# Kernel optimization log

Hardware: AMD Instinct MI355X
Metric: run time of the kernel (lower is better)

Reference implementation:

```python
import jax, jax.numpy as jnp
import numpy as np

DIM = 512
HEADS = 16
DHEAD = DIM // HEADS
SQRT_DIM = float(np.sqrt(DIM))


def sinusoidal_pe(length, dim):
    # Transformer-XL style sinusoidal positional embedding, shape (length, dim)
    pos = jnp.arange(length, dtype=jnp.float32)[:, None]
    i = jnp.arange(0, dim, 2, dtype=jnp.float32)
    div = jnp.exp(-(jnp.log(jnp.float32(10000.0)) * i / dim))[None, :]
    ang = pos * div
    pe = jnp.zeros((length, dim), dtype=jnp.float32)
    pe = pe.at[:, 0::2].set(jnp.sin(ang)).at[:, 1::2].set(jnp.cos(ang))
    return pe


def rel_shift(x):
    # x: (B, H, L, M) -> Transformer-XL relative shift
    B, H, L, M = x.shape
    x = jnp.concatenate([jnp.zeros((B, H, L, 1), x.dtype), x], axis=-1)  # (B,H,L,M+1)
    x = x.reshape(B, H, M + 1, L)[:, :, 1:, :].reshape(B, H, L, M)
    return x


def setup_inputs() -> dict:
    key = jax.random.key(0)
    ks = jax.random.split(key, 16)
    B, L = 8, 1024
    s = 0.02
    return {
        "query": jax.random.normal(ks[0], (B, L, DIM), jnp.float32),
        "key_in": jax.random.normal(ks[1], (B, L, DIM), jnp.float32),
        "value": jax.random.normal(ks[2], (B, L, DIM), jnp.float32),
        "Wq": jax.random.normal(ks[3], (DIM, DIM), jnp.float32) * s,
        "bq": jnp.zeros((DIM,), jnp.float32),
        "Wk": jax.random.normal(ks[4], (DIM, DIM), jnp.float32) * s,
        "bk": jnp.zeros((DIM,), jnp.float32),
        "Wv": jax.random.normal(ks[5], (DIM, DIM), jnp.float32) * s,
        "bv": jnp.zeros((DIM,), jnp.float32),
        "Wpos": jax.random.normal(ks[6], (DIM, DIM), jnp.float32) * s,
        "u_bias": jax.random.normal(ks[7], (HEADS, DHEAD), jnp.float32) * s,
        "v_bias": jax.random.normal(ks[8], (HEADS, DHEAD), jnp.float32) * s,
        "Wo": jax.random.normal(ks[9], (DIM, DIM), jnp.float32) * s,
        "bo": jnp.zeros((DIM,), jnp.float32),
    }


def reference(query, key_in, value, Wq, bq, Wk, bk, Wv, bv, Wpos, u_bias, v_bias, Wo, bo):
    B, L, _ = value.shape
    pe = sinusoidal_pe(L, DIM)                                   # (L, dim)
    q = (query @ Wq.T + bq).reshape(B, L, HEADS, DHEAD)          # (B,L,H,d)
    k = (key_in @ Wk.T + bk).reshape(B, L, HEADS, DHEAD)         # (B,L,H,d)
    v = (value @ Wv.T + bv).reshape(B, L, HEADS, DHEAD)          # (B,L,H,d)
    pos = (pe @ Wpos.T).reshape(L, HEADS, DHEAD)                 # (L,H,d)

    content_score = jnp.einsum("blhd,bmhd->bhlm", q + u_bias, k)
    pos_score = jnp.einsum("blhd,mhd->bhlm", q + v_bias, pos)
    pos_score = rel_shift(pos_score)
    score = (content_score + pos_score) / SQRT_DIM               # (B,H,L,L)
    attn = jax.nn.softmax(score, axis=-1)
    context = jnp.einsum("bhlm,bmhd->blhd", attn, v).reshape(B, L, DIM)
    return context @ Wo.T + bo
```

## Files before the change

kernel.cpp:

```cpp
#include <hip/hip_runtime.h>
#include <hip/hip_bf16.h>
#include <cstddef>

typedef _Float16 f16;
typedef _Float16 f16x8 __attribute__((ext_vector_type(8)));
typedef _Float16 f16x4 __attribute__((ext_vector_type(4)));
typedef _Float16 f16x2 __attribute__((ext_vector_type(2)));
typedef float    f32x4 __attribute__((ext_vector_type(4)));

#define MFMA16(a,b,c) __builtin_amdgcn_mfma_f32_16x16x32_f16((a),(b),(c),0,0,0)

__device__ __forceinline__ void gload16(const void* g, void* lds) {
  __builtin_amdgcn_global_load_lds((const __attribute__((address_space(1))) void*)g,
                                   (__attribute__((address_space(3))) void*)lds, 16, 0, 0);
}

__global__ __launch_bounds__(256) void conv_w(
    const float* __restrict__ w0, const float* __restrict__ w1,
    const float* __restrict__ w2, const float* __restrict__ w3,
    const float* __restrict__ w4, f16* __restrict__ dst)
{
  const int idx = blockIdx.x * 256 + threadIdx.x;
  const int seg = idx >> 16;
  const int r   = idx & 65535;
  const float* s = seg == 0 ? w0 : seg == 1 ? w1 : seg == 2 ? w2 : seg == 3 ? w3 : w4;
  float4 v = ((const float4*)s)[r];
  f16x4 h = { (f16)v.x, (f16)v.y, (f16)v.z, (f16)v.w };
  ((f16x4*)(dst + ((size_t)seg << 18)))[r] = h;
}

__global__ __launch_bounds__(256) void pe16_kernel(f16* __restrict__ pe) {
  const int l = blockIdx.x;
  const int p = threadIdx.x;
  const float divv = expf(-(logf(10000.0f) * (2.0f * (float)p)) / 512.0f);
  const float ang  = (float)l * divv;
  f16x2 o = { (f16)sinf(ang), (f16)cosf(ang) };
  *(f16x2*)(pe + (size_t)l * 512 + 2 * p) = o;
}

__global__ __launch_bounds__(256) void gemm128_qkv(
    const float* __restrict__ q_in, const float* __restrict__ k_in,
    const float* __restrict__ v_in, const f16* __restrict__ W16,
    const float* __restrict__ bq, const float* __restrict__ bk,
    const float* __restrict__ bv,
    f16* __restrict__ Qf, f16* __restrict__ Kf, f16* __restrict__ Vtf)
{
  __shared__ __align__(16) char Asm[16384];
  __shared__ __align__(16) char Bsm[16384];

  const int z = blockIdx.z;
  const float* Ap   = z == 0 ? q_in : z == 1 ? k_in : v_in;
  const f16*   Wf   = W16 + (size_t)z * 262144;
  const float* bias = z == 0 ? bq : z == 1 ? bk : bv;
  f16*         Cp   = z == 0 ? Qf : z == 1 ? Kf : Vtf;

  const int tid   = threadIdx.x;
  const int gm0   = blockIdx.x * 128;
  const int gn0   = blockIdx.y * 128;
  const int lane  = tid & 63, w = tid >> 6;
  const int row16 = lane & 15, grp = lane >> 4;
  const int wm = w & 1, wn = w >> 1;
  const int lr8  = lane >> 3;
  const int swcb = ((lane & 7) ^ lr8) * 16;

  f32x4 acc[4][4];
#pragma unroll
  for (int i = 0; i < 4; ++i)
#pragma unroll
    for (int j = 0; j < 4; ++j)
#pragma unroll
      for (int r = 0; r < 4; ++r) acc[i][j][r] = 0.f;

  for (int k0 = 0; k0 < 512; k0 += 64) {
    __syncthreads();
    float4 areg[8];
#pragma unroll
    for (int i = 0; i < 8; ++i) {
      const int u = tid + i * 256;
      const int row = u >> 4, cf = (u & 15) * 4;
      areg[i] = *(const float4*)(Ap + (size_t)(gm0 + row) * 512 + k0 + cf);
    }
#pragma unroll
    for (int i = 0; i < 4; ++i) {
      const int rB = w * 32 + i * 8;
      gload16((const char*)Wf + ((size_t)(gn0 + rB + lr8)) * 1024 + (size_t)k0 * 2 + swcb,
              Bsm + rB * 128);
    }
#pragma unroll
    for (int i = 0; i < 8; ++i) {
      const int u = tid + i * 256;
      const int row = u >> 4, cf = (u & 15) * 4;
      f16x4 hv = { (f16)areg[i].x, (f16)areg[i].y, (f16)areg[i].z, (f16)areg[i].w };
      *(f16x4*)(Asm + row * 128 + ((cf * 2) ^ ((row & 7) * 16))) = hv;
    }
    asm volatile("s_waitcnt vmcnt(0)" ::: "memory");
    __syncthreads();
#pragma unroll
    for (int kk = 0; kk < 64; kk += 32) {
      const int cb = (kk + 8 * grp) * 2;
      f16x8 af[4], bf[4];
#pragma unroll
      for (int f = 0; f < 4; ++f) {
        const int ra = wm * 64 + f * 16 + row16;
        const int rb = wn * 64 + f * 16 + row16;
        af[f] = *(const f16x8*)(Asm + ra * 128 + (cb ^ ((ra & 7) * 16)));
        bf[f] = *(const f16x8*)(Bsm + rb * 128 + (cb ^ ((rb & 7) * 16)));
      }
#pragma unroll
      for (int fi = 0; fi < 4; ++fi)
#pragma unroll
        for (int fj = 0; fj < 4; ++fj)
          acc[fi][fj] = MFMA16(af[fi], bf[fj], acc[fi][fj]);
    }
  }

#pragma unroll
  for (int fi = 0; fi < 4; ++fi)
#pragma unroll
    for (int fj = 0; fj < 4; ++fj) {
      const int gc = gn0 + wn * 64 + fj * 16 + row16;
      const float bval = bias[gc];
#pragma unroll
      for (int r = 0; r < 4; ++r) {
        const int gr = gm0 + wm * 64 + fi * 16 + grp * 4 + r;
        const float v = acc[fi][fj][r] + bval;
        const int b = gr >> 10, l = gr & 1023, h = gc >> 5, d = gc & 31;
        if (z != 2) {
          Cp[(((size_t)(b * 16 + h)) * 1024 + l) * 32 + d] = (f16)v;
        } else {
          Cp[(((size_t)(b * 16 + h)) * 32 + d) * 1024 + l] = (f16)v;
        }
      }
    }
}

template<int MODE>
__global__ __launch_bounds__(256) void gemm128_f16(
    const f16* __restrict__ Ap, const f16* __restrict__ Wf,
    const float* __restrict__ bias, void* __restrict__ Cp)
{
  __shared__ __align__(16) char Asm[16384];
  __shared__ __align__(16) char Bsm[16384];

  const int tid   = threadIdx.x;
  const int gm0   = blockIdx.x * 128;
  const int gn0   = blockIdx.y * 128;
  const int lane  = tid & 63, w = tid >> 6;
  const int row16 = lane & 15, grp = lane >> 4;
  const int wm = w & 1, wn = w >> 1;
  const int lr8  = lane >> 3;
  const int swcb = ((lane & 7) ^ lr8) * 16;

  f32x4 acc[4][4];
#pragma unroll
  for (int i = 0; i < 4; ++i)
#pragma unroll
    for (int j = 0; j < 4; ++j)
#pragma unroll
      for (int r = 0; r < 4; ++r) acc[i][j][r] = 0.f;

  for (int k0 = 0; k0 < 512; k0 += 64) {
    __syncthreads();
#pragma unroll
    for (int i = 0; i < 4; ++i) {
      const int rr = w * 32 + i * 8;
      gload16((const char*)Ap + ((size_t)(gm0 + rr + lr8)) * 1024 + (size_t)k0 * 2 + swcb,
              Asm + rr * 128);
      gload16((const char*)Wf + ((size_t)(gn0 + rr + lr8)) * 1024 + (size_t)k0 * 2 + swcb,
              Bsm + rr * 128);
    }
    asm volatile("s_waitcnt vmcnt(0)" ::: "memory");
    __syncthreads();
#pragma unroll
    for (int kk = 0; kk < 64; kk += 32) {
      const int cb = (kk + 8 * grp) * 2;
      f16x8 af[4], bf[4];
#pragma unroll
      for (int f = 0; f < 4; ++f) {
        const int ra = wm * 64 + f * 16 + row16;
        const int rb = wn * 64 + f * 16 + row16;
        af[f] = *(const f16x8*)(Asm + ra * 128 + (cb ^ ((ra & 7) * 16)));
        bf[f] = *(const f16x8*)(Bsm + rb * 128 + (cb ^ ((rb & 7) * 16)));
      }
#pragma unroll
      for (int fi = 0; fi < 4; ++fi)
#pragma unroll
        for (int fj = 0; fj < 4; ++fj)
          acc[fi][fj] = MFMA16(af[fi], bf[fj], acc[fi][fj]);
    }
  }

#pragma unroll
  for (int fi = 0; fi < 4; ++fi)
#pragma unroll
    for (int fj = 0; fj < 4; ++fj) {
      const int gc = gn0 + wn * 64 + fj * 16 + row16;
      float bval;
      if constexpr (MODE == 2) bval = 0.f; else bval = bias[gc];
#pragma unroll
      for (int r = 0; r < 4; ++r) {
        const int gr = gm0 + wm * 64 + fi * 16 + grp * 4 + r;
        const float v = acc[fi][fj][r] + bval;
        if constexpr (MODE == 2) {
          const int h = gc >> 5, d = gc & 31;
          ((f16*)Cp)[(((size_t)h) * 1024 + gr) * 32 + d] = (f16)v;
        } else {
          ((float*)Cp)[(size_t)gr * 512 + gc] = v;
        }
      }
    }
}

__global__ __launch_bounds__(256) void attn_kernel(
    const f16* __restrict__ Qf, const f16* __restrict__ Kf,
    const f16* __restrict__ Vt, const f16* __restrict__ Pos,
    const float* __restrict__ ubias, const float* __restrict__ vbias,
    f16* __restrict__ ctx)
{
  __shared__ f16 P_lds[17][1028];
  __shared__ f16 ptile[4][16][72];

  const int tid   = threadIdx.x;
  const int w     = tid >> 6, lane = tid & 63;
  const int row16 = lane & 15, grp = lane >> 4;
  const int b = blockIdx.z, h = blockIdx.y;
  const int l0 = blockIdx.x * 16;

  const size_t bh = (size_t)(b * 16 + h);
  const f16* Qb = Qf + bh * 1024 * 32;
  const f16* Kb = Kf + bh * 1024 * 32;
  const f16* Vb = Vt + bh * 32 * 1024;
  const f16* Pb = Pos + (size_t)h * 1024 * 32;

  const f32x4 z4 = {0.f, 0.f, 0.f, 0.f};
  const float scale = 0.04419417382f;

  f16x8 qu, qv, qv2;
  {
    f16x8 qraw = *(const f16x8*)(Qb + (size_t)(l0 + row16) * 32 + 8 * grp);
    const int r2 = l0 + 16 + row16;
    f16x8 q2 = *(const f16x8*)(Qb + (size_t)(r2 < 1024 ? r2 : 1023) * 32 + 8 * grp);
#pragma unroll
    for (int e = 0; e < 8; ++e) {
      const float u = ubias[h * 32 + 8 * grp + e];
      const float v = vbias[h * 32 + 8 * grp + e];
      qu[e]  = (f16)((float)qraw[e] + u);
      qv[e]  = (f16)((float)qraw[e] + v);
      qv2[e] = (f16)((float)q2[e]   + v);
    }
  }

  if (tid < 17) {
    f16x4 z = {(f16)0.f, (f16)0.f, (f16)0.f, (f16)0.f};
    *(f16x4*)&P_lds[tid][1024] = z;
  }

#pragma unroll 4
  for (int c = 0; c < 16; ++c) {
    const int jc = w * 16 + c;
    f16x8 pf = *(const f16x8*)(Pb + (size_t)(jc * 16 + row16) * 32 + 8 * grp);
    f32x4 p0 = MFMA16(pf, qv,  z4);
    f32x4 p1 = MFMA16(pf, qv2, z4);
    const int j0 = jc * 16 + grp * 4;
    {
      f16x4 vv = { (f16)(p0[0] * scale), (f16)(p0[1] * scale),
                   (f16)(p0[2] * scale), (f16)(p0[3] * scale) };
      *(f16x4*)&P_lds[row16][j0] = vv;
    }
    if (row16 == 0) {
      f16x4 vv = { (f16)(p1[0] * scale), (f16)(p1[1] * scale),
                   (f16)(p1[2] * scale), (f16)(p1[3] * scale) };
      *(f16x4*)&P_lds[16][j0] = vv;
    }
  }
  __syncthreads();

  float psum = 0.f;
  f32x4 od[2];
#pragma unroll
  for (int hh = 0; hh < 2; ++hh) for (int r = 0; r < 4; ++r) od[hh][r] = 0.f;

  const int  c1   = 1023 - l0 - row16;
  const f16* Prow = &P_lds[row16][0];

  for (int ti = 0; ti < 4; ++ti) {
    const int mbase = w * 256 + ti * 64;
    f32x4 st[4];
#pragma unroll
    for (int c = 0; c < 4; ++c) {
      f16x8 kf = *(const f16x8*)(Kb + (size_t)(mbase + c * 16 + row16) * 32 + 8 * grp);
      st[c] = MFMA16(kf, qu, z4);
    }
#pragma unroll
    for (int c = 0; c < 4; ++c) {
      float p[4];
#pragma unroll
      for (int r = 0; r < 4; ++r) {
        const int jA  = mbase + c * 16 + grp * 4 + r + c1;
        const int idx = jA + (jA >= 1025 ? 3 : 0);
        const float sh = (float)Prow[idx];
        const float s  = fmaf(st[c][r], scale, sh);
        p[r] = __expf(s);
        psum += p[r];
      }
      f16x4 pv = { (f16)p[0], (f16)p[1], (f16)p[2], (f16)p[3] };
      *(f16x4*)&ptile[w][row16][c * 16 + grp * 4] = pv;
    }
#pragma unroll
    for (int kc = 0; kc < 2; ++kc) {
      f16x8 pa = *(const f16x8*)&ptile[w][row16][kc * 32 + 8 * grp];
#pragma unroll
      for (int hh = 0; hh < 2; ++hh) {
        f16x8 vf = *(const f16x8*)(Vb + (size_t)(hh * 16 + row16) * 1024 + mbase + kc * 32 + 8 * grp);
        od[hh] = MFMA16(pa, vf, od[hh]);
      }
    }
  }

  float l1 = psum + __shfl_xor(psum, 16);
  l1 += __shfl_xor(l1, 32);

  __syncthreads();
  float* mo = (float*)&P_lds[0][0];
  float* ls = mo + 4 * 16 * 32;
#pragma unroll
  for (int hh = 0; hh < 2; ++hh)
#pragma unroll
    for (int r = 0; r < 4; ++r)
      mo[(w * 16 + grp * 4 + r) * 32 + hh * 16 + row16] = od[hh][r];
  if (grp == 0) ls[w * 16 + row16] = l1;
  __syncthreads();

  const int q = tid >> 4, dp = tid & 15;
  const float Ls = ls[q] + ls[16 + q] + ls[32 + q] + ls[48 + q];
  float o0 = 0.f, o1 = 0.f;
#pragma unroll
  for (int ww = 0; ww < 4; ++ww) {
    o0 += mo[(ww * 16 + q) * 32 + 2 * dp];
    o1 += mo[(ww * 16 + q) * 32 + 2 * dp + 1];
  }
  const float inv = 1.f / Ls;
  const size_t oidx = ((size_t)(b * 1024 + l0 + q)) * 512 + h * 32 + 2 * dp;
  f16x2 o2 = { (f16)(o0 * inv), (f16)(o1 * inv) };
  *(f16x2*)(ctx + oidx) = o2;
}

extern "C" void kernel_launch(void* const* d_in, const int* in_sizes, int n_in,
                              void* d_out, int out_size, void* d_ws, size_t ws_size,
                              hipStream_t stream) {
  const float* query  = (const float*)d_in[0];
  const float* key_in = (const float*)d_in[1];
  const float* value  = (const float*)d_in[2];
  const float* Wq = (const float*)d_in[3];
  const float* bq = (const float*)d_in[4];
  const float* Wk = (const float*)d_in[5];
  const float* bk = (const float*)d_in[6];
  const float* Wv = (const float*)d_in[7];
  const float* bv = (const float*)d_in[8];
  const float* Wpos = (const float*)d_in[9];
  const float* ub   = (const float*)d_in[10];
  const float* vb   = (const float*)d_in[11];
  const float* Wo = (const float*)d_in[12];
  const float* bo = (const float*)d_in[13];
  float* out = (float*)d_out;

  char* ws = (char*)d_ws;
  f16* W16  = (f16*)(ws);
  f16* pe16 = (f16*)(ws + 2621440);
  f16* Qf   = (f16*)(ws + 3670016);
  f16* Kf   = (f16*)(ws + 12058624);
  f16* Vtf  = (f16*)(ws + 20447232);
  f16* Pf   = (f16*)(ws + 28835840);
  f16* ctx  = (f16*)(ws + 29884416);

  conv_w<<<1280, 256, 0, stream>>>(Wq, Wk, Wv, Wpos, Wo, W16);
  pe16_kernel<<<1024, 256, 0, stream>>>(pe16);
  gemm128_qkv<<<dim3(64, 4, 3), 256, 0, stream>>>(query, key_in, value, W16,
                                                  bq, bk, bv, Qf, Kf, Vtf);
  gemm128_f16<2><<<dim3(8,  4), 256, 0, stream>>>(pe16, W16 + 786432, nullptr, Pf);
  attn_kernel<<<dim3(64, 16, 8), 256, 0, stream>>>(Qf, Kf, Vtf, Pf, ub, vb, ctx);
  gemm128_f16<3><<<dim3(64, 4), 256, 0, stream>>>(ctx, W16 + 1048576, bo, out);
}
```

Measured before the change: 319.5 us.

## Merge prep and projection launches; pass attention P tile via shuffles

Merges the weight-conversion and positional-encoding kernels into one launch, and folds the positional projection GEMM into the QKV projection kernel as a fourth z-slice that exits early for unused blocks. This cuts the launch count from six to four. In the attention kernel, the softmax probability tile now moves from the accumulator layout to the MFMA A-operand layout with cross-lane shuffles instead of an LDS round-trip, which removes the ptile shared buffer and lowers LDS use per block. The cost is extra shuffle and select instructions, plus a grid slice of mostly idle blocks.

New measurement: 340.6 us. 1.07x slower.

```diff
diff --git a/kernel.cpp b/kernel.cpp
--- a/kernel.cpp
+++ b/kernel.cpp
@@ -15,44 +15,49 @@
                                    (__attribute__((address_space(3))) void*)lds, 16, 0, 0);
 }
 
-__global__ __launch_bounds__(256) void conv_w(
+__global__ __launch_bounds__(256) void prep_kernel(
     const float* __restrict__ w0, const float* __restrict__ w1,
     const float* __restrict__ w2, const float* __restrict__ w3,
-    const float* __restrict__ w4, f16* __restrict__ dst)
+    const float* __restrict__ w4, f16* __restrict__ dst,
+    f16* __restrict__ pe)
 {
-  const int idx = blockIdx.x * 256 + threadIdx.x;
-  const int seg = idx >> 16;
-  const int r   = idx & 65535;
-  const float* s = seg == 0 ? w0 : seg == 1 ? w1 : seg == 2 ? w2 : seg == 3 ? w3 : w4;
-  float4 v = ((const float4*)s)[r];
-  f16x4 h = { (f16)v.x, (f16)v.y, (f16)v.z, (f16)v.w };
-  ((f16x4*)(dst + ((size_t)seg << 18)))[r] = h;
-}
-
-__global__ __launch_bounds__(256) void pe16_kernel(f16* __restrict__ pe) {
-  const int l = blockIdx.x;
-  const int p = threadIdx.x;
-  const float divv = expf(-(logf(10000.0f) * (2.0f * (float)p)) / 512.0f);
-  const float ang  = (float)l * divv;
-  f16x2 o = { (f16)sinf(ang), (f16)cosf(ang) };
-  *(f16x2*)(pe + (size_t)l * 512 + 2 * p) = o;
-}
-
-__global__ __launch_bounds__(256) void gemm128_qkv(
+  if (blockIdx.x < 1280) {
+    const int idx = blockIdx.x * 256 + threadIdx.x;
+    const int seg = idx >> 16;
+    const int r   = idx & 65535;
+    const float* s = seg == 0 ? w0 : seg == 1 ? w1 : seg == 2 ? w2 : seg == 3 ? w3 : w4;
+    float4 v = ((const float4*)s)[r];
+    f16x4 h = { (f16)v.x, (f16)v.y, (f16)v.z, (f16)v.w };
+    ((f16x4*)(dst + ((size_t)seg << 18)))[r] = h;
+  } else {
+    const int l = blockIdx.x - 1280;
+    const int p = threadIdx.x;
+    const float divv = expf(-(logf(10000.0f) * (2.0f * (float)p)) / 512.0f);
+    const float ang  = (float)l * divv;
+    f16x2 o = { (f16)sinf(ang), (f16)cosf(ang) };
+    *(f16x2*)(pe + (size_t)l * 512 + 2 * p) = o;
+  }
+}
+
+__global__ __launch_bounds__(256) void gemm_main(
     const float* __restrict__ q_in, const float* __restrict__ k_in,
-    const float* __restrict__ v_in, const f16* __restrict__ W16,
+    const float* __restrict__ v_in, const f16* __restrict__ pe16,
+    const f16* __restrict__ W16,
     const float* __restrict__ bq, const float* __restrict__ bk,
     const float* __restrict__ bv,
-    f16* __restrict__ Qf, f16* __restrict__ Kf, f16* __restrict__ Vtf)
+    f16* __restrict__ Qf, f16* __restrict__ Kf, f16* __restrict__ Vtf,
+    f16* __restrict__ Pf)
 {
+  const int z = blockIdx.z;
+  if (z == 3 && blockIdx.x >= 8) return;
+
   __shared__ __align__(16) char Asm[16384];
   __shared__ __align__(16) char Bsm[16384];
 
-  const int z = blockIdx.z;
   const float* Ap   = z == 0 ? q_in : z == 1 ? k_in : v_in;
   const f16*   Wf   = W16 + (size_t)z * 262144;
-  const float* bias = z == 0 ? bq : z == 1 ? bk : bv;
-  f16*         Cp   = z == 0 ? Qf : z == 1 ? Kf : Vtf;
+  const float* bias = z == 0 ? bq : z == 1 ? bk : z == 2 ? bv : nullptr;
+  f16*         Cp   = z == 0 ? Qf : z == 1 ? Kf : z == 2 ? Vtf : Pf;
 
   const int tid   = threadIdx.x;
   const int gm0   = blockIdx.x * 128;
@@ -74,11 +79,20 @@
   for (int k0 = 0; k0 < 512; k0 += 64) {
     __syncthreads();
     float4 areg[8];
-#pragma unroll
-    for (int i = 0; i < 8; ++i) {
-      const int u = tid + i * 256;
-      const int row = u >> 4, cf = (u & 15) * 4;
-      areg[i] = *(const float4*)(Ap + (size_t)(gm0 + row) * 512 + k0 + cf);
+    if (z != 3) {
+#pragma unroll
+      for (int i = 0; i < 8; ++i) {
+        const int u = tid + i * 256;
+        const int row = u >> 4, cf = (u & 15) * 4;
+        areg[i] = *(const float4*)(Ap + (size_t)(gm0 + row) * 512 + k0 + cf);
+      }
+    } else {
+#pragma unroll
+      for (int i = 0; i < 4; ++i) {
+        const int rA = w * 32 + i * 8;
+        gload16((const char*)pe16 + ((size_t)(gm0 + rA + lr8)) * 1024 + (size_t)k0 * 2 + swcb,
+                Asm + rA * 128);
+      }
     }
 #pragma unroll
     for (int i = 0; i < 4; ++i) {
@@ -86,12 +100,14 @@
       gload16((const char*)Wf + ((size_t)(gn0 + rB + lr8)) * 1024 + (size_t)k0 * 2 + swcb,
               Bsm + rB * 128);
     }
-#pragma unroll
-    for (int i = 0; i < 8; ++i) {
-      const int u = tid + i * 256;
-      const int row = u >> 4, cf = (u & 15) * 4;
-      f16x4 hv = { (f16)areg[i].x, (f16)areg[i].y, (f16)areg[i].z, (f16)areg[i].w };
-      *(f16x4*)(Asm + row * 128 + ((cf * 2) ^ ((row & 7) * 16))) = hv;
+    if (z != 3) {
+#pragma unroll
+      for (int i = 0; i < 8; ++i) {
+        const int u = tid + i * 256;
+        const int row = u >> 4, cf = (u & 15) * 4;
+        f16x4 hv = { (f16)areg[i].x, (f16)areg[i].y, (f16)areg[i].z, (f16)areg[i].w };
+        *(f16x4*)(Asm + row * 128 + ((cf * 2) ^ ((row & 7) * 16))) = hv;
+      }
     }
     asm volatile("s_waitcnt vmcnt(0)" ::: "memory");
     __syncthreads();
@@ -119,25 +135,29 @@
 #pragma unroll
     for (int fj = 0; fj < 4; ++fj) {
       const int gc = gn0 + wn * 64 + fj * 16 + row16;
-      const float bval = bias[gc];
+      const float bval = (z == 3) ? 0.f : bias[gc];
 #pragma unroll
       for (int r = 0; r < 4; ++r) {
         const int gr = gm0 + wm * 64 + fi * 16 + grp * 4 + r;
         const float v = acc[fi][fj][r] + bval;
-        const int b = gr >> 10, l = gr & 1023, h = gc >> 5, d = gc & 31;
-        if (z != 2) {
-          Cp[(((size_t)(b * 16 + h)) * 1024 + l) * 32 + d] = (f16)v;
+        const int h = gc >> 5, d = gc & 31;
+        if (z == 3) {
+          Cp[(((size_t)h) * 1024 + gr) * 32 + d] = (f16)v;
         } else {
-          Cp[(((size_t)(b * 16 + h)) * 32 + d) * 1024 + l] = (f16)v;
+          const int b = gr >> 10, l = gr & 1023;
+          if (z != 2) {
+            Cp[(((size_t)(b * 16 + h)) * 1024 + l) * 32 + d] = (f16)v;
+          } else {
+            Cp[(((size_t)(b * 16 + h)) * 32 + d) * 1024 + l] = (f16)v;
+          }
         }
       }
     }
 }
 
-template<int MODE>
-__global__ __launch_bounds__(256) void gemm128_f16(
+__global__ __launch_bounds__(256) void gemm_out(
     const f16* __restrict__ Ap, const f16* __restrict__ Wf,
-    const float* __restrict__ bias, void* __restrict__ Cp)
+    const float* __restrict__ bias, float* __restrict__ Cp)
 {
   __shared__ __align__(16) char Asm[16384];
   __shared__ __align__(16) char Bsm[16384];
@@ -195,18 +215,11 @@
 #pragma unroll
     for (int fj = 0; fj < 4; ++fj) {
       const int gc = gn0 + wn * 64 + fj * 16 + row16;
-      float bval;
-      if constexpr (MODE == 2) bval = 0.f; else bval = bias[gc];
+      const float bval = bias[gc];
 #pragma unroll
       for (int r = 0; r < 4; ++r) {
         const int gr = gm0 + wm * 64 + fi * 16 + grp * 4 + r;
-        const float v = acc[fi][fj][r] + bval;
-        if constexpr (MODE == 2) {
-          const int h = gc >> 5, d = gc & 31;
-          ((f16*)Cp)[(((size_t)h) * 1024 + gr) * 32 + d] = (f16)v;
-        } else {
-          ((float*)Cp)[(size_t)gr * 512 + gc] = v;
-        }
+        Cp[(size_t)gr * 512 + gc] = acc[fi][fj][r] + bval;
       }
     }
 }
@@ -218,7 +231,6 @@
     f16* __restrict__ ctx)
 {
   __shared__ f16 P_lds[17][1028];
-  __shared__ f16 ptile[4][16][72];
 
   const int tid   = threadIdx.x;
   const int w     = tid >> 6, lane = tid & 63;
@@ -282,6 +294,8 @@
 
   const int  c1   = 1023 - l0 - row16;
   const f16* Prow = &P_lds[row16][0];
+  const int  sbase = row16 + ((grp & 1) << 5);
+  const bool hiG   = (grp & 2) != 0;
 
   for (int ti = 0; ti < 4; ++ti) {
     const int mbase = w * 256 + ti * 64;
@@ -291,6 +305,8 @@
       f16x8 kf = *(const f16x8*)(Kb + (size_t)(mbase + c * 16 + row16) * 32 + 8 * grp);
       st[c] = MFMA16(kf, qu, z4);
     }
+
+    unsigned X[4][2];
 #pragma unroll
     for (int c = 0; c < 4; ++c) {
       float p[4];
@@ -303,16 +319,26 @@
         p[r] = __expf(s);
         psum += p[r];
       }
-      f16x4 pv = { (f16)p[0], (f16)p[1], (f16)p[2], (f16)p[3] };
-      *(f16x4*)&ptile[w][row16][c * 16 + grp * 4] = pv;
-    }
+      f16x2 t0 = { (f16)p[0], (f16)p[1] };
+      f16x2 t1 = { (f16)p[2], (f16)p[3] };
+      X[c][0] = __builtin_bit_cast(unsigned, t0);
+      X[c][1] = __builtin_bit_cast(unsigned, t1);
+    }
+
 #pragma unroll
     for (int kc = 0; kc < 2; ++kc) {
-      f16x8 pa = *(const f16x8*)&ptile[w][row16][kc * 32 + 8 * grp];
+      union { unsigned u[4]; f16x8 v; } pa;
+#pragma unroll
+      for (int wd = 0; wd < 4; ++wd) {
+        const int src = sbase + ((wd >> 1) << 4);
+        const unsigned lo = (unsigned)__shfl((int)X[2 * kc][wd & 1], src, 64);
+        const unsigned hi = (unsigned)__shfl((int)X[2 * kc + 1][wd & 1], src, 64);
+        pa.u[wd] = hiG ? hi : lo;
+      }
 #pragma unroll
       for (int hh = 0; hh < 2; ++hh) {
         f16x8 vf = *(const f16x8*)(Vb + (size_t)(hh * 16 + row16) * 1024 + mbase + kc * 32 + 8 * grp);
-        od[hh] = MFMA16(pa, vf, od[hh]);
+        od[hh] = MFMA16(pa.v, vf, od[hh]);
       }
     }
   }
@@ -373,11 +399,9 @@
   f16* Pf   = (f16*)(ws + 28835840);
   f16* ctx  = (f16*)(ws + 29884416);
 
-  conv_w<<<1280, 256, 0, stream>>>(Wq, Wk, Wv, Wpos, Wo, W16);
-  pe16_kernel<<<1024, 256, 0, stream>>>(pe16);
-  gemm128_qkv<<<dim3(64, 4, 3), 256, 0, stream>>>(query, key_in, value, W16,
-                                                  bq, bk, bv, Qf, Kf, Vtf);
-  gemm128_f16<2><<<dim3(8,  4), 256, 0, stream>>>(pe16, W16 + 786432, nullptr, Pf);
+  prep_kernel<<<2304, 256, 0, stream>>>(Wq, Wk, Wv, Wpos, Wo, W16, pe16);
+  gemm_main<<<dim3(64, 4, 4), 256, 0, stream>>>(query, key_in, value, pe16, W16,
+                                                bq, bk, bv, Qf, Kf, Vtf, Pf);
   attn_kernel<<<dim3(64, 16, 8), 256, 0, stream>>>(Qf, Kf, Vtf, Pf, ub, vb, ctx);
-  gemm128_f16<3><<<dim3(64, 4), 256, 0, stream>>>(ctx, W16 + 1048576, bo, out);
-}
+  gemm_out<<<dim3(64, 4), 256, 0, stream>>>(ctx, W16 + 1048576, bo, out);
+}
```

## Use exp2 with folded log2e, register shuffles instead of LDS ptile, uniform shift paths

Applied to the files above, without the earlier changes.

Folds log2(e) into the score scale so softmax uses the hardware exp2 instruction directly. Replaces the per-wave LDS ptile round trip, used to re-layout P from the MFMA output layout to the A-operand layout, with cross-lane shuffles. Splits the rel_shift lookup into branch-free uniform paths for tiles entirely above or below the diagonal and keeps the general path only for boundary tiles. It also fully unrolls the tile loop, which adds register pressure and instruction count.

Result: faster. 309.8 us (-3.0%).

```diff
diff --git a/kernel.cpp b/kernel.cpp
--- a/kernel.cpp
+++ b/kernel.cpp
@@ -9,6 +9,12 @@
 typedef float    f32x4 __attribute__((ext_vector_type(4)));
 
 #define MFMA16(a,b,c) __builtin_amdgcn_mfma_f32_16x16x32_f16((a),(b),(c),0,0,0)
+
+#if __has_builtin(__builtin_amdgcn_exp2f)
+#define EXP2(x) __builtin_amdgcn_exp2f(x)
+#else
+#define EXP2(x) __expf((x) * 0.6931471805599453f)
+#endif
 
 __device__ __forceinline__ void gload16(const void* g, void* lds) {
   __builtin_amdgcn_global_load_lds((const __attribute__((address_space(1))) void*)g,
@@ -218,7 +224,6 @@
     f16* __restrict__ ctx)
 {
   __shared__ f16 P_lds[17][1028];
-  __shared__ f16 ptile[4][16][72];
 
   const int tid   = threadIdx.x;
   const int w     = tid >> 6, lane = tid & 63;
@@ -233,7 +238,7 @@
   const f16* Pb = Pos + (size_t)h * 1024 * 32;
 
   const f32x4 z4 = {0.f, 0.f, 0.f, 0.f};
-  const float scale = 0.04419417382f;
+  const float kpre = 0.0637587157f;
 
   f16x8 qu, qv, qv2;
   {
@@ -263,13 +268,13 @@
     f32x4 p1 = MFMA16(pf, qv2, z4);
     const int j0 = jc * 16 + grp * 4;
     {
-      f16x4 vv = { (f16)(p0[0] * scale), (f16)(p0[1] * scale),
-                   (f16)(p0[2] * scale), (f16)(p0[3] * scale) };
+      f16x4 vv = { (f16)(p0[0] * kpre), (f16)(p0[1] * kpre),
+                   (f16)(p0[2] * kpre), (f16)(p0[3] * kpre) };
       *(f16x4*)&P_lds[row16][j0] = vv;
     }
     if (row16 == 0) {
-      f16x4 vv = { (f16)(p1[0] * scale), (f16)(p1[1] * scale),
-                   (f16)(p1[2] * scale), (f16)(p1[3] * scale) };
+      f16x4 vv = { (f16)(p1[0] * kpre), (f16)(p1[1] * kpre),
+                   (f16)(p1[2] * kpre), (f16)(p1[3] * kpre) };
       *(f16x4*)&P_lds[16][j0] = vv;
     }
   }
@@ -280,9 +285,12 @@
 #pragma unroll
   for (int hh = 0; hh < 2; ++hh) for (int r = 0; r < 4; ++r) od[hh][r] = 0.f;
 
-  const int  c1   = 1023 - l0 - row16;
-  const f16* Prow = &P_lds[row16][0];
-
+  const f16* vA = &P_lds[0][0] + row16 * 1028 + w * 256 + (1023 - l0 - row16) + 4 * grp;
+  const f16* vB = vA + 3;
+  const int  sbase = row16 + ((grp & 1) << 5);
+  const bool hiG   = (grp & 2) != 0;
+
+#pragma unroll
   for (int ti = 0; ti < 4; ++ti) {
     const int mbase = w * 256 + ti * 64;
     f32x4 st[4];
@@ -291,28 +299,61 @@
       f16x8 kf = *(const f16x8*)(Kb + (size_t)(mbase + c * 16 + row16) * 32 + 8 * grp);
       st[c] = MFMA16(kf, qu, z4);
     }
+
+    float sh[4][4];
+    const bool unifB = (mbase >= l0 + 17);
+    const bool unifA = (mbase + 62 <= l0);
+    if (unifB) {
+#pragma unroll
+      for (int c = 0; c < 4; ++c)
+#pragma unroll
+        for (int r = 0; r < 4; ++r) sh[c][r] = (float)vB[ti * 64 + c * 16 + r];
+    } else if (unifA) {
+#pragma unroll
+      for (int c = 0; c < 4; ++c)
+#pragma unroll
+        for (int r = 0; r < 4; ++r) sh[c][r] = (float)vA[ti * 64 + c * 16 + r];
+    } else {
+      const int c1 = 1023 - l0 - row16;
+      const f16* Prow = &P_lds[row16][0];
+#pragma unroll
+      for (int c = 0; c < 4; ++c)
+#pragma unroll
+        for (int r = 0; r < 4; ++r) {
+          const int jA = mbase + c * 16 + grp * 4 + r + c1;
+          sh[c][r] = (float)Prow[jA + (jA >= 1025 ? 3 : 0)];
+        }
+    }
+
+    unsigned X[4][2];
 #pragma unroll
     for (int c = 0; c < 4; ++c) {
       float p[4];
 #pragma unroll
       for (int r = 0; r < 4; ++r) {
-        const int jA  = mbase + c * 16 + grp * 4 + r + c1;
-        const int idx = jA + (jA >= 1025 ? 3 : 0);
-        const float sh = (float)Prow[idx];
-        const float s  = fmaf(st[c][r], scale, sh);
-        p[r] = __expf(s);
+        p[r] = EXP2(fmaf(st[c][r], kpre, sh[c][r]));
         psum += p[r];
       }
-      f16x4 pv = { (f16)p[0], (f16)p[1], (f16)p[2], (f16)p[3] };
-      *(f16x4*)&ptile[w][row16][c * 16 + grp * 4] = pv;
-    }
+      f16x2 t0 = { (f16)p[0], (f16)p[1] };
+      f16x2 t1 = { (f16)p[2], (f16)p[3] };
+      X[c][0] = __builtin_bit_cast(unsigned, t0);
+      X[c][1] = __builtin_bit_cast(unsigned, t1);
+    }
+
 #pragma unroll
     for (int kc = 0; kc < 2; ++kc) {
-      f16x8 pa = *(const f16x8*)&ptile[w][row16][kc * 32 + 8 * grp];
+      union { unsigned u[4]; f16x8 v; } pa;
+#pragma unroll
+      for (int wd = 0; wd < 4; ++wd) {
+        const int src = sbase + ((wd >> 1) << 4);
+        const unsigned lo = (unsigned)__shfl((int)X[2 * kc][wd & 1], src, 64);
+        const unsigned hi = (unsigned)__shfl((int)X[2 * kc + 1][wd & 1], src, 64);
+        pa.u[wd] = hiG ? hi : lo;
+      }
 #pragma unroll
       for (int hh = 0; hh < 2; ++hh) {
         f16x8 vf = *(const f16x8*)(Vb + (size_t)(hh * 16 + row16) * 1024 + mbase + kc * 32 + 8 * grp);
-        od[hh] = MFMA16(pa, vf, od[hh]);
+        od[hh] = MFMA16(pa.v, vf, od[hh]);
       }
     }
   }
```
